# Kernel tuning notes

Measured on AMD Instinct MI355X. Metric: run time of the kernel, lower is better.

The kernel has to match this reference:

```python
import jax, jax.numpy as jnp
import numpy as np

N, E = 50000, 800000
IN_DIM, HID, HEADS, OUT_DIM, NUM_CLASSES = 512, 128, 4, 64, 4


def setup_inputs() -> dict:
    key = jax.random.key(0)
    ks = jax.random.split(key, 18)
    g = lambda k, shape, s=0.05: (jax.random.normal(k, shape, dtype=jnp.float32) * s)
    x = jax.random.normal(ks[0], (N, IN_DIM), dtype=jnp.float32)
    edge_index = jax.random.randint(ks[1], (2, E), 0, N, dtype=jnp.int32)
    return {
        "x": x,
        "edge_index": edge_index,
        # GATConv layer 1 (heads=4, concat)
        "W1": g(ks[2], (IN_DIM, HEADS * HID)),
        "att_src1": g(ks[3], (HEADS, HID)),
        "att_dst1": g(ks[4], (HEADS, HID)),
        "b1": jnp.zeros((HEADS * HID,), jnp.float32),
        # GATConv layer 2 (heads=1, no concat)
        "W2": g(ks[5], (HEADS * HID, OUT_DIM)),
        "att_src2": g(ks[6], (1, OUT_DIM)),
        "att_dst2": g(ks[7], (1, OUT_DIM)),
        "b2": jnp.zeros((OUT_DIM,), jnp.float32),
        # intra_attention MLP: Linear(out,out) -> tanh -> Linear(out,1) -> softmax(dim=0)
        "Wa": g(ks[8], (OUT_DIM, OUT_DIM)),
        "ba": jnp.zeros((OUT_DIM,), jnp.float32),
        "wv": g(ks[9], (OUT_DIM, 1)),
        "bv": jnp.zeros((1,), jnp.float32),
        "class_attn": g(ks[10], (NUM_CLASSES, OUT_DIM), 0.3),
        # classifier
        "Wc": g(ks[11], (OUT_DIM, NUM_CLASSES)),
        "bc": jnp.zeros((NUM_CLASSES,), jnp.float32),
    }


def _gat_layer(x, src, dst, W, att_src, att_dst, heads, feat):
    """PyG GATConv: gather -> LeakyReLU score -> segment softmax -> scatter add."""
    n = x.shape[0]
    h = (x @ W).reshape(n, heads, feat)                     # [N,H,F]
    a_s = jnp.sum(h * att_src[None], axis=-1)               # [N,H]
    a_d = jnp.sum(h * att_dst[None], axis=-1)               # [N,H]
    e = jax.nn.leaky_relu(a_s[src] + a_d[dst], 0.2)         # [E,H]
    m = jax.ops.segment_max(e, dst, num_segments=n)         # per-dst max
    ex = jnp.exp(e - m[dst])
    s = jax.ops.segment_sum(ex, dst, num_segments=n)
    alpha = ex / (s[dst] + 1e-16)                           # [E,H]
    msg = h[src] * alpha[:, :, None]                        # [E,H,F]
    return jax.ops.segment_sum(msg, dst, num_segments=n)    # [N,H,F]


def reference(x, edge_index, W1, att_src1, att_dst1, b1, W2, att_src2, att_dst2,
              b2, Wa, ba, wv, bv, class_attn, Wc, bc):
    n = x.shape[0]
    loop = jnp.arange(n, dtype=edge_index.dtype)
    src = jnp.concatenate([edge_index[0], loop])            # add_self_loops=True
    dst = jnp.concatenate([edge_index[1], loop])

    h1 = _gat_layer(x, src, dst, W1, att_src1, att_dst1, HEADS, HID)
    h1 = h1.reshape(n, HEADS * HID) + b1                    # concat heads + bias
    h1 = jax.nn.elu(h1)

    h2 = _gat_layer(h1, src, dst, W2, att_src2, att_dst2, 1, OUT_DIM)
    h2 = h2.reshape(n, OUT_DIM) + b2                        # heads=1, concat=False

    # intra-sample attention, softmax over nodes (dim=0)
    scores = jnp.tanh(h2 @ Wa + ba) @ wv + bv               # [N,1]
    attw = jax.nn.softmax(scores, axis=0)
    xw = h2 * attw                                          # [N,OUT]

    xn = xw / jnp.maximum(jnp.linalg.norm(xw, axis=1, keepdims=True), 1e-12)
    cn = class_attn / jnp.maximum(
        jnp.linalg.norm(class_attn, axis=1, keepdims=True), 1e-12)
    inter_class_scores = xn @ cn.T                          # [N,C]

    out = xw @ Wc + bc                                      # [N,C]
    return out, xw, inter_class_scores
```

## Files before the change

kernel.cpp:

```cpp
#include <hip/hip_runtime.h>
#include <cstdint>
#include <cstddef>

typedef __attribute__((ext_vector_type(8))) short bf16x8;
typedef __attribute__((ext_vector_type(4))) float f32x4;
typedef __attribute__((ext_vector_type(8))) unsigned short u16x8;

__device__ __forceinline__ unsigned encf(float f) {
  unsigned u = __float_as_uint(f);
  return (u & 0x80000000u) ? ~u : (u | 0x80000000u);
}
__device__ __forceinline__ float decf(unsigned u) {
  return (u & 0x80000000u) ? __uint_as_float(u & 0x7FFFFFFFu) : __uint_as_float(~u);
}
__device__ __forceinline__ float lrelu02(float x) { return x > 0.f ? x : 0.2f * x; }
__device__ __forceinline__ unsigned short f2bf(float f) {
  unsigned u = __float_as_uint(f);
  unsigned r = u + 0x7FFFu + ((u >> 16) & 1u);
  return (unsigned short)(r >> 16);
}
__device__ __forceinline__ float bf2f(unsigned short b) {
  return __uint_as_float(((unsigned)b) << 16);
}

__device__ __forceinline__ void gll16(const void* g, void* l) {
  __builtin_amdgcn_global_load_lds(
      (const __attribute__((address_space(1))) void*)g,
      (__attribute__((address_space(3))) void*)l, 16, 0, 0);
}

__global__ void zero_int_k(int* __restrict__ p, int n) {
  int i = blockIdx.x * 256 + threadIdx.x;
  if (i < n) p[i] = 0;
}

__global__ void hist_k(const int* __restrict__ ei, int E, int N, int* __restrict__ counts) {
  int i = blockIdx.x * 256 + threadIdx.x;
  int Eall = E + N;
  if (i >= Eall) return;
  int dst = (i < E) ? ei[E + i] : (i - E);
  atomicAdd(&counts[dst], 1);
}

__global__ __launch_bounds__(256) void scan1_k(const int* __restrict__ counts,
                                               int* __restrict__ incl,
                                               int* __restrict__ bsum, int N) {
  int b = blockIdx.x, tid = threadIdx.x;
  int lane = tid & 63, wv = tid >> 6;
  int i = b * 256 + tid;
  int v = (i < N) ? counts[i] : 0;
#pragma unroll
  for (int o = 1; o < 64; o <<= 1) {
    int t = __shfl_up(v, o, 64);
    if (lane >= o) v += t;
  }
  __shared__ int wsum[4];
  if (lane == 63) wsum[wv] = v;
  __syncthreads();
  int base = 0;
  for (int wj = 0; wj < wv; wj++) base += wsum[wj];
  v += base;
  if (i < N) incl[i] = v;
  if (tid == 255) bsum[b] = v;
}

__global__ __launch_bounds__(256) void scan2_k(const int* __restrict__ bsum,
                                               int* __restrict__ pb, int nb) {
  int tid = threadIdx.x;
  int lane = tid & 63, wv = tid >> 6;
  int v = (tid < nb) ? bsum[tid] : 0;
  int orig = v;
#pragma unroll
  for (int o = 1; o < 64; o <<= 1) {
    int t = __shfl_up(v, o, 64);
    if (lane >= o) v += t;
  }
  __shared__ int wsum[4];
  if (lane == 63) wsum[wv] = v;
  __syncthreads();
  int base = 0;
  for (int wj = 0; wj < wv; wj++) base += wsum[wj];
  if (tid < nb) pb[tid] = v + base - orig;
}

__global__ void scan3_k(const int* __restrict__ incl, const int* __restrict__ pb,
                        int* __restrict__ offs, int* __restrict__ cursor, int N) {
  int i = blockIdx.x * 256 + threadIdx.x;
  if (i == 0) { offs[0] = 0; cursor[0] = 0; }
  if (i < N) {
    int v = incl[i] + pb[i >> 8];
    offs[i + 1] = v;
    if (i + 1 < N) cursor[i + 1] = v;
  }
}

__global__ void scatter_k(const int* __restrict__ ei, int E, int N,
                          int* __restrict__ cursor, int* __restrict__ ssrc) {
  int i = blockIdx.x * 256 + threadIdx.x;
  int Eall = E + N;
  if (i >= Eall) return;
  int src, dst;
  if (i < E) { src = ei[i]; dst = ei[E + i]; }
  else       { src = i - E; dst = i - E; }
  int pos = atomicAdd(&cursor[dst], 1);
  ssrc[pos] = src;
}

__global__ void conv_x_k(const float* __restrict__ x, unsigned short* __restrict__ xb,
                         int N, int Mpad) {
  int i = blockIdx.x * 256 + threadIdx.x;
  int total = Mpad * 64;
  if (i >= total) return;
  int row = i >> 6;
  u16x8 v;
  if (row < N) {
    const float4* src = (const float4*)(x + (size_t)i * 8);
    float4 a = src[0], b = src[1];
    v[0] = f2bf(a.x); v[1] = f2bf(a.y); v[2] = f2bf(a.z); v[3] = f2bf(a.w);
    v[4] = f2bf(b.x); v[5] = f2bf(b.y); v[6] = f2bf(b.z); v[7] = f2bf(b.w);
  } else {
    v = (u16x8)0;
  }
  *(u16x8*)(xb + (size_t)i * 8) = v;
}

__global__ void conv_wt_k(const float* __restrict__ W, unsigned short* __restrict__ Wt,
                          int K, int Nc) {
  int i = blockIdx.x * 256 + threadIdx.x;
  if (i >= K * Nc) return;
  int c = i / K, k = i - c * K;
  Wt[i] = f2bf(W[(size_t)k * Nc + c]);
}

template <int BM, int BN, bool OBF, bool DOTS>
__global__ __launch_bounds__(256) void mfma_gemm_k(const unsigned short* __restrict__ A,
                                                   const unsigned short* __restrict__ Bt,
                                                   void* __restrict__ Cv,
                                                   const float* __restrict__ att_s,
                                                   const float* __restrict__ att_d,
                                                   float* __restrict__ as_out,
                                                   float* __restrict__ ad_out,
                                                   int M, int K, int Nc) {
  constexpr int BK = 64;
  constexpr int MR = BM / 32;
  constexpr int NR = BN / 32;
  __shared__ unsigned short As[BM][BK];
  __shared__ unsigned short Bs[BN][BK];
  const int tid = threadIdx.x;
  const int lane = tid & 63;
  const int w = tid >> 6;
  const int wr = w >> 1, wc = w & 1;
  const int l16 = lane & 15, lk = lane >> 4;
  const int row0 = blockIdx.x * BM, col0 = blockIdx.y * BN;

  f32x4 acc[MR][NR];
#pragma unroll
  for (int m = 0; m < MR; m++)
#pragma unroll
    for (int n = 0; n < NR; n++) acc[m][n] = (f32x4)0.f;

  const char* Abase = (const char*)A;
  const char* Bbase = (const char*)Bt;

  for (int k0 = 0; k0 < K; k0 += BK) {
#pragma unroll
    for (int i = 0; i < BM / 32; i++) {
      int ca = i * 256 + tid;
      int r = ca >> 3, b = (ca & 7) * 16;
      gll16(Abase + ((size_t)(row0 + r) * K + k0) * 2 + b, (char*)&As[0][0] + ca * 16);
    }
#pragma unroll
    for (int i = 0; i < BN / 32; i++) {
      int cb = i * 256 + tid;
      int c = cb >> 3, b = (cb & 7) * 16;
      gll16(Bbase + ((size_t)(col0 + c) * K + k0) * 2 + b, (char*)&Bs[0][0] + cb * 16);
    }
    __syncthreads();
#pragma unroll
    for (int ks = 0; ks < 2; ks++) {
      bf16x8 af[MR], bfr[NR];
#pragma unroll
      for (int m = 0; m < MR; m++)
        af[m] = *(const bf16x8*)&As[wr * (BM / 2) + m * 16 + l16][ks * 32 + lk * 8];
#pragma unroll
      for (int n = 0; n < NR; n++)
        bfr[n] = *(const bf16x8*)&Bs[wc * (BN / 2) + n * 16 + l16][ks * 32 + lk * 8];
#pragma unroll
      for (int m = 0; m < MR; m++)
#pragma unroll
        for (int n = 0; n < NR; n++)
          acc[m][n] = __builtin_amdgcn_mfma_f32_16x16x32_bf16(af[m], bfr[n], acc[m][n], 0, 0, 0);
    }
    __syncthreads();
  }
#pragma unroll
  for (int m = 0; m < MR; m++) {
    int row_b = row0 + wr * (BM / 2) + m * 16 + lk * 4;
#pragma unroll
    for (int r = 0; r < 4; r++) {
      int row = row_b + r;
      if (row < M) {
#pragma unroll
        for (int n = 0; n < NR; n++) {
          int col = col0 + wc * (BN / 2) + n * 16 + l16;
          if (OBF)
            ((unsigned short*)Cv)[(size_t)row * Nc + col] = f2bf(acc[m][n][r]);
          else
            ((float*)Cv)[(size_t)row * Nc + col] = acc[m][n][r];
        }
      }
    }
  }
  if constexpr (DOTS) {
    __shared__ float s_ds[2][BM];
    __shared__ float s_dd[2][BM];
    float as_c[NR], ad_c[NR];
#pragma unroll
    for (int n = 0; n < NR; n++) {
      int col = col0 + wc * (BN / 2) + n * 16 + l16;
      as_c[n] = att_s[col];
      ad_c[n] = att_d[col];
    }
#pragma unroll
    for (int m = 0; m < MR; m++) {
#pragma unroll
      for (int r = 0; r < 4; r++) {
        float ps = 0.f, pd = 0.f;
#pragma unroll
        for (int n = 0; n < NR; n++) {
          ps += acc[m][n][r] * as_c[n];
          pd += acc[m][n][r] * ad_c[n];
        }
#pragma unroll
        for (int o = 8; o; o >>= 1) { ps += __shfl_xor(ps, o); pd += __shfl_xor(pd, o); }
        if (l16 == 0) {
          int rr = wr * (BM / 2) + m * 16 + lk * 4 + r;
          s_ds[wc][rr] = ps;
          s_dd[wc][rr] = pd;
        }
      }
    }
    __syncthreads();
    if (tid < BM) {
      int row = row0 + tid;
      if (row < M) {
        as_out[(size_t)row * 4 + blockIdx.y] = s_ds[0][tid] + s_ds[1][tid];
        ad_out[(size_t)row * 4 + blockIdx.y] = s_dd[0][tid] + s_dd[1][tid];
      }
    }
  }
}

__global__ __launch_bounds__(256) void attn_dots2_k(const float* __restrict__ h,
                                                    const float* __restrict__ att_s,
                                                    const float* __restrict__ att_d,
                                                    float* __restrict__ a_s,
                                                    float* __restrict__ a_d, int N) {
  int lane = threadIdx.x & 63, wave = threadIdx.x >> 6;
  int n = blockIdx.x * 4 + wave;
  if (n >= N) return;
  float v = h[(size_t)n * 64 + lane];
  float ps = v * att_s[lane], pd = v * att_d[lane];
#pragma unroll
  for (int o = 32; o; o >>= 1) { ps += __shfl_xor(ps, o); pd += __shfl_xor(pd, o); }
  if (lane == 0) { a_s[n] = ps; a_d[n] = pd; }
}

__global__ __launch_bounds__(256) void gat_agg1_k(const unsigned short* __restrict__ hfeat,
                                                  const float* __restrict__ a_s,
                                                  const float* __restrict__ a_d,
                                                  const int* __restrict__ offs,
                                                  const int* __restrict__ ssrc,
                                                  const float* __restrict__ b1,
                                                  unsigned short* __restrict__ h1b, int N) {
  const int tid = threadIdx.x;
  const int lane = tid & 63, wave = tid >> 6;
  const int n = blockIdx.x * 4 + wave;
  if (n >= N) return;
  __shared__ int   s_src[4][64];
  __shared__ float s_ex[4][64][4];
  const int start = offs[n], end = offs[n + 1];
  const int hhl = lane >> 4;
  const float4 adv4 = *(const float4*)(a_d + (size_t)n * 4);
  const float4* as4 = (const float4*)a_s;

  float m0 = -1e30f, m1 = -1e30f, m2 = -1e30f, m3 = -1e30f;
  float S0 = 0.f, S1 = 0.f, S2 = 0.f, S3 = 0.f;
  float acc[8] = {0.f, 0.f, 0.f, 0.f, 0.f, 0.f, 0.f, 0.f};

  for (int base = start; base < end; base += 64) {
    const int cnt = min(64, end - base);
    float e0 = -1e30f, e1 = -1e30f, e2 = -1e30f, e3 = -1e30f;
    int s = 0;
    if (lane < cnt) {
      s = ssrc[base + lane];
      float4 av = as4[s];
      e0 = lrelu02(av.x + adv4.x);
      e1 = lrelu02(av.y + adv4.y);
      e2 = lrelu02(av.z + adv4.z);
      e3 = lrelu02(av.w + adv4.w);
    }
    float c0 = e0, c1 = e1, c2 = e2, c3 = e3;
#pragma unroll
    for (int o = 32; o; o >>= 1) {
      c0 = fmaxf(c0, __shfl_xor(c0, o));
      c1 = fmaxf(c1, __shfl_xor(c1, o));
      c2 = fmaxf(c2, __shfl_xor(c2, o));
      c3 = fmaxf(c3, __shfl_xor(c3, o));
    }
    float nm0 = fmaxf(m0, c0), nm1 = fmaxf(m1, c1);
    float nm2 = fmaxf(m2, c2), nm3 = fmaxf(m3, c3);
    float sc0 = __expf(m0 - nm0), sc1 = __expf(m1 - nm1);
    float sc2 = __expf(m2 - nm2), sc3 = __expf(m3 - nm3);
    m0 = nm0; m1 = nm1; m2 = nm2; m3 = nm3;
    float x0 = (lane < cnt) ? __expf(e0 - nm0) : 0.f;
    float x1 = (lane < cnt) ? __expf(e1 - nm1) : 0.f;
    float x2 = (lane < cnt) ? __expf(e2 - nm2) : 0.f;
    float x3 = (lane < cnt) ? __expf(e3 - nm3) : 0.f;
    s_src[wave][lane] = s;
    s_ex[wave][lane][0] = x0; s_ex[wave][lane][1] = x1;
    s_ex[wave][lane][2] = x2; s_ex[wave][lane][3] = x3;
#pragma unroll
    for (int o = 32; o; o >>= 1) {
      x0 += __shfl_xor(x0, o); x1 += __shfl_xor(x1, o);
      x2 += __shfl_xor(x2, o); x3 += __shfl_xor(x3, o);
    }
    S0 = S0 * sc0 + x0; S1 = S1 * sc1 + x1;
    S2 = S2 * sc2 + x2; S3 = S3 * sc3 + x3;
    float scl = (hhl == 0) ? sc0 : (hhl == 1) ? sc1 : (hhl == 2) ? sc2 : sc3;
#pragma unroll
    for (int q = 0; q < 8; q++) acc[q] *= scl;
#pragma unroll 4
    for (int j = 0; j < cnt; j++) {
      int sj = s_src[wave][j];
      float al = s_ex[wave][j][hhl];
      uint4 pk = *(const uint4*)(hfeat + ((size_t)sj << 9) + lane * 8);
      acc[0] += al * __uint_as_float(pk.x << 16);
      acc[1] += al * __uint_as_float(pk.x & 0xFFFF0000u);
      acc[2] += al * __uint_as_float(pk.y << 16);
      acc[3] += al * __uint_as_float(pk.y & 0xFFFF0000u);
      acc[4] += al * __uint_as_float(pk.z << 16);
      acc[5] += al * __uint_as_float(pk.z & 0xFFFF0000u);
      acc[6] += al * __uint_as_float(pk.w << 16);
      acc[7] += al * __uint_as_float(pk.w & 0xFFFF0000u);
    }
  }
  float inv = 1.f / (((hhl == 0) ? S0 : (hhl == 1) ? S1 : (hhl == 2) ? S2 : S3) + 1e-16f);
  const float4 b1a = *(const float4*)(b1 + lane * 8);
  const float4 b1b = *(const float4*)(b1 + lane * 8 + 4);
  float v[8];
  v[0] = acc[0] * inv + b1a.x; v[1] = acc[1] * inv + b1a.y;
  v[2] = acc[2] * inv + b1a.z; v[3] = acc[3] * inv + b1a.w;
  v[4] = acc[4] * inv + b1b.x; v[5] = acc[5] * inv + b1b.y;
  v[6] = acc[6] * inv + b1b.z; v[7] = acc[7] * inv + b1b.w;
  u16x8 outv;
#pragma unroll
  for (int q = 0; q < 8; q++) {
    float t = v[q] > 0.f ? v[q] : (__expf(v[q]) - 1.f);
    outv[q] = f2bf(t);
  }
  *(u16x8*)(h1b + ((size_t)n << 9) + lane * 8) = outv;
}

__global__ __launch_bounds__(256) void gat_agg2_k(const float* __restrict__ h2pre,
                                                  const float* __restrict__ a_s,
                                                  const float* __restrict__ a_d,
                                                  const int* __restrict__ offs,
                                                  const int* __restrict__ ssrc,
                                                  const float* __restrict__ b2,
                                                  float* __restrict__ h2out, int N) {
  const int tid = threadIdx.x;
  const int lane = tid & 63, wave = tid >> 6;
  const int n = blockIdx.x * 4 + wave;
  if (n >= N) return;
  __shared__ int   s_src[4][64];
  __shared__ float s_ex[4][64];
  const int start = offs[n], end = offs[n + 1];
  const float ad = a_d[n];

  float m = -1e30f, S = 0.f, acc = 0.f;
  for (int base = start; base < end; base += 64) {
    const int cnt = min(64, end - base);
    float e = -1e30f;
    int s = 0;
    if (lane < cnt) {
      s = ssrc[base + lane];
      e = lrelu02(a_s[s] + ad);
    }
    float c = e;
#pragma unroll
    for (int o = 32; o; o >>= 1) c = fmaxf(c, __shfl_xor(c, o));
    float nm = fmaxf(m, c);
    float sc = __expf(m - nm);
    m = nm;
    float x = (lane < cnt) ? __expf(e - nm) : 0.f;
    s_src[wave][lane] = s;
    s_ex[wave][lane] = x;
#pragma unroll
    for (int o = 32; o; o >>= 1) x += __shfl_xor(x, o);
    S = S * sc + x;
    acc *= sc;
#pragma unroll 4
    for (int j = 0; j < cnt; j++) {
      int sj = s_src[wave][j];
      float al = s_ex[wave][j];
      acc += al * h2pre[((size_t)sj << 6) + lane];
    }
  }
  h2out[((size_t)n << 6) + lane] = acc / (S + 1e-16f) + b2[lane];
}

__global__ __launch_bounds__(256) void score_k(const float* __restrict__ h2,
                                               const float* __restrict__ Wa,
                                               const float* __restrict__ ba,
                                               const float* __restrict__ wv,
                                               const float* __restrict__ bv,
                                               float* __restrict__ scores, int N) {
  int lane = threadIdx.x & 63, wave = threadIdx.x >> 6;
  int n = blockIdx.x * 4 + wave;
  if (n >= N) return;
  float hv = h2[(size_t)n * 64 + lane];
  float t = ba[lane];
  for (int k = 0; k < 64; k++) {
    float hk = __shfl(hv, k);
    t += hk * Wa[k * 64 + lane];
  }
  t = tanhf(t);
  float p = t * wv[lane];
#pragma unroll
  for (int o = 32; o; o >>= 1) p += __shfl_xor(p, o);
  if (lane == 0) scores[n] = p + bv[0];
}

__global__ void red_init_k(unsigned* __restrict__ red) {
  if (threadIdx.x == 0) { red[0] = 0x007FFFFFu; red[1] = 0u; }
}

__global__ void score_max_k(const float* __restrict__ scores, unsigned* __restrict__ red, int N) {
  int i = blockIdx.x * 256 + threadIdx.x;
  float m = (i < N) ? scores[i] : -1e30f;
#pragma unroll
  for (int o = 32; o; o >>= 1) m = fmaxf(m, __shfl_xor(m, o));
  if ((threadIdx.x & 63) == 0) atomicMax(&red[0], encf(m));
}

__global__ void score_sum_k(const float* __restrict__ scores, unsigned* __restrict__ red, int N) {
  float M = decf(red[0]);
  int i = blockIdx.x * 256 + threadIdx.x;
  float s = (i < N) ? __expf(scores[i] - M) : 0.f;
#pragma unroll
  for (int o = 32; o; o >>= 1) s += __shfl_xor(s, o);
  if ((threadIdx.x & 63) == 0) atomicAdd(reinterpret_cast<float*>(red) + 1, s);
}

__global__ void prep_cn_k(const float* __restrict__ ca, float* __restrict__ cn) {
  int lane = threadIdx.x & 63, c = threadIdx.x >> 6;
  float v = ca[c * 64 + lane];
  float p = v * v;
#pragma unroll
  for (int o = 32; o; o >>= 1) p += __shfl_xor(p, o);
  cn[c * 64 + lane] = v / fmaxf(sqrtf(p), 1e-12f);
}

__global__ __launch_bounds__(256) void finalize_k(const float* __restrict__ h2,
                                                  const float* __restrict__ scores,
                                                  const unsigned* __restrict__ red,
                                                  const float* __restrict__ cn,
                                                  const float* __restrict__ Wc,
                                                  const float* __restrict__ bc,
                                                  float* __restrict__ out, int N) {
  int lane = threadIdx.x & 63, wave = threadIdx.x >> 6;
  int n = blockIdx.x * 4 + wave;
  if (n >= N) return;
  float M = decf(red[0]);
  float S = __uint_as_float(red[1]);
  float attw = __expf(scores[n] - M) / S;
  float xw = h2[(size_t)n * 64 + lane] * attw;
  float p = xw * xw;
#pragma unroll
  for (int o = 32; o; o >>= 1) p += __shfl_xor(p, o);
  float xn = xw / fmaxf(sqrtf(p), 1e-12f);
  float i0 = xn * cn[lane],       i1 = xn * cn[64 + lane];
  float i2 = xn * cn[128 + lane], i3 = xn * cn[192 + lane];
  float o0 = xw * Wc[lane * 4 + 0], o1 = xw * Wc[lane * 4 + 1];
  float o2 = xw * Wc[lane * 4 + 2], o3 = xw * Wc[lane * 4 + 3];
#pragma unroll
  for (int o = 32; o; o >>= 1) {
    i0 += __shfl_xor(i0, o); i1 += __shfl_xor(i1, o);
    i2 += __shfl_xor(i2, o); i3 += __shfl_xor(i3, o);
    o0 += __shfl_xor(o0, o); o1 += __shfl_xor(o1, o);
    o2 += __shfl_xor(o2, o); o3 += __shfl_xor(o3, o);
  }
  float* outp   = out;
  float* xwp    = out + (size_t)N * 4;
  float* interp = out + (size_t)N * 68;
  xwp[(size_t)n * 64 + lane] = xw;
  if (lane == 0) {
    outp[n * 4 + 0] = o0 + bc[0]; outp[n * 4 + 1] = o1 + bc[1];
    outp[n * 4 + 2] = o2 + bc[2]; outp[n * 4 + 3] = o3 + bc[3];
    interp[n * 4 + 0] = i0; interp[n * 4 + 1] = i1;
    interp[n * 4 + 2] = i2; interp[n * 4 + 3] = i3;
  }
}

extern "C" void kernel_launch(void* const* d_in, const int* in_sizes, int n_in,
                              void* d_out, int out_size, void* d_ws, size_t ws_size,
                              hipStream_t stream) {
  const float* x        = (const float*)d_in[0];
  const int*   ei       = (const int*)d_in[1];
  const float* W1       = (const float*)d_in[2];
  const float* att_src1 = (const float*)d_in[3];
  const float* att_dst1 = (const float*)d_in[4];
  const float* b1       = (const float*)d_in[5];
  const float* W2       = (const float*)d_in[6];
  const float* att_src2 = (const float*)d_in[7];
  const float* att_dst2 = (const float*)d_in[8];
  const float* b2       = (const float*)d_in[9];
  const float* Wa       = (const float*)d_in[10];
  const float* ba       = (const float*)d_in[11];
  const float* wv       = (const float*)d_in[12];
  const float* bv       = (const float*)d_in[13];
  const float* class_attn = (const float*)d_in[14];
  const float* Wc       = (const float*)d_in[15];
  const float* bc       = (const float*)d_in[16];

  const int N = in_sizes[0] / 512;
  const int E = in_sizes[1] / 2;
  const int Eall = E + N;
  const int Mpad = ((N + 127) / 128) * 128;
  const int nb = (N + 255) / 256;

  char* w = (char*)d_ws;
  size_t off = 0;
  auto alloc = [&](size_t bytes) -> void* {
    off = (off + 255) & ~((size_t)255);
    void* p = w + off;
    off += bytes;
    return p;
  };
  unsigned short* xb  = (unsigned short*)alloc((size_t)Mpad * 512 * 2);
  unsigned short* h1b = xb;
  unsigned short* hb  = (unsigned short*)alloc((size_t)N * 512 * 2);
  float* h2pre  = (float*)alloc((size_t)N * 64 * 4);
  float* h2     = (float*)alloc((size_t)N * 64 * 4);
  unsigned short* W1t = (unsigned short*)alloc((size_t)512 * 512 * 2);
  unsigned short* W2t = (unsigned short*)alloc((size_t)64 * 512 * 2);
  float* as1    = (float*)alloc((size_t)N * 4 * 4);
  float* ad1    = (float*)alloc((size_t)N * 4 * 4);
  float* as2    = (float*)alloc((size_t)N * 4);
  float* ad2    = (float*)alloc((size_t)N * 4);
  int*   counts = (int*)alloc((size_t)N * 4);
  int*   incl   = (int*)alloc((size_t)N * 4);
  int*   bsum   = (int*)alloc(256 * 4);
  int*   pb     = (int*)alloc(256 * 4);
  int*   offs   = (int*)alloc((size_t)(N + 1) * 4);
  int*   cursor = (int*)alloc((size_t)N * 4);
  int*   ssrc   = (int*)alloc((size_t)Eall * 4);
  float* scores = (float*)alloc((size_t)N * 4);
  unsigned* red = (unsigned*)alloc(64);
  float* cn     = (float*)alloc(256 * 4);

  const int gN256  = (N + 255) / 256;
  const int gE256  = (Eall + 255) / 256;
  const int gNode4 = (N + 3) / 4;

  zero_int_k<<<gN256, 256, 0, stream>>>(counts, N);
  hist_k<<<gE256, 256, 0, stream>>>(ei, E, N, counts);
  scan1_k<<<nb, 256, 0, stream>>>(counts, incl, bsum, N);
  scan2_k<<<1, 256, 0, stream>>>(bsum, pb, nb);
  scan3_k<<<gN256, 256, 0, stream>>>(incl, pb, offs, cursor, N);
  scatter_k<<<gE256, 256, 0, stream>>>(ei, E, N, cursor, ssrc);

  conv_x_k<<<(Mpad * 64 + 255) / 256, 256, 0, stream>>>(x, xb, N, Mpad);
  conv_wt_k<<<(512 * 512 + 255) / 256, 256, 0, stream>>>(W1, W1t, 512, 512);
  conv_wt_k<<<(64 * 512 + 255) / 256, 256, 0, stream>>>(W2, W2t, 512, 64);

  mfma_gemm_k<128, 128, true, true><<<dim3(Mpad / 128, 4), 256, 0, stream>>>(
      xb, W1t, hb, att_src1, att_dst1, as1, ad1, N, 512, 512);
  gat_agg1_k<<<gNode4, 256, 0, stream>>>(hb, as1, ad1, offs, ssrc, b1, h1b, N);

  mfma_gemm_k<64, 64, false, false><<<dim3(Mpad / 64, 1), 256, 0, stream>>>(
      h1b, W2t, h2pre, nullptr, nullptr, nullptr, nullptr, N, 512, 64);
  attn_dots2_k<<<gNode4, 256, 0, stream>>>(h2pre, att_src2, att_dst2, as2, ad2, N);
  gat_agg2_k<<<gNode4, 256, 0, stream>>>(h2pre, as2, ad2, offs, ssrc, b2, h2, N);

  score_k<<<gNode4, 256, 0, stream>>>(h2, Wa, ba, wv, bv, scores, N);
  red_init_k<<<1, 64, 0, stream>>>(red);
  score_max_k<<<gN256, 256, 0, stream>>>(scores, red, N);
  score_sum_k<<<gN256, 256, 0, stream>>>(scores, red, N);
  prep_cn_k<<<1, 256, 0, stream>>>(class_attn, cn);
  finalize_k<<<gNode4, 256, 0, stream>>>(h2, scores, red, cn, Wc, bc,
                                         (float*)d_out, N);
}
```

Baseline: 481.6 us.

## Widen GEMM1 tile, fuse layer-2 attention dots into GEMM2, store h2 in bf16

GEMM1 now uses a 128x256 tile, so each block covers two heads and writes per-head dot products directly, halving the grid's column dimension and reusing A tiles more. GEMM2 gets a specialised kernel that computes the att_src/att_dst dots in its epilogue, which removes the separate attn_dots2 pass. It also writes h2pre as bf16, and gat_agg2 splits edges across wave halves with packed bf16 pair loads. This cuts gather bandwidth in the second aggregation, at the cost of bf16 rounding of h2pre and higher register and LDS use in GEMM1.

```diff
diff --git a/kernel.cpp b/kernel.cpp
--- a/kernel.cpp
+++ b/kernel.cpp
@@ -132,45 +132,43 @@
   Wt[i] = f2bf(W[(size_t)k * Nc + c]);
 }
 
-template <int BM, int BN, bool OBF, bool DOTS>
-__global__ __launch_bounds__(256) void mfma_gemm_k(const unsigned short* __restrict__ A,
-                                                   const unsigned short* __restrict__ Bt,
-                                                   void* __restrict__ Cv,
-                                                   const float* __restrict__ att_s,
-                                                   const float* __restrict__ att_d,
-                                                   float* __restrict__ as_out,
-                                                   float* __restrict__ ad_out,
-                                                   int M, int K, int Nc) {
-  constexpr int BK = 64;
-  constexpr int MR = BM / 32;
-  constexpr int NR = BN / 32;
-  __shared__ unsigned short As[BM][BK];
-  __shared__ unsigned short Bs[BN][BK];
+__global__ __launch_bounds__(256, 2) void gemm1_k(const unsigned short* __restrict__ A,
+                                                  const unsigned short* __restrict__ Bt,
+                                                  unsigned short* __restrict__ C,
+                                                  const float* __restrict__ att_s,
+                                                  const float* __restrict__ att_d,
+                                                  float* __restrict__ as_out,
+                                                  float* __restrict__ ad_out,
+                                                  int M, int K, int Nc) {
+  __shared__ unsigned short As[128][64];
+  __shared__ unsigned short Bs[256][64];
+  __shared__ float s_ds[2][128];
+  __shared__ float s_dd[2][128];
   const int tid = threadIdx.x;
   const int lane = tid & 63;
   const int w = tid >> 6;
   const int wr = w >> 1, wc = w & 1;
   const int l16 = lane & 15, lk = lane >> 4;
-  const int row0 = blockIdx.x * BM, col0 = blockIdx.y * BN;
-
-  f32x4 acc[MR][NR];
-#pragma unroll
-  for (int m = 0; m < MR; m++)
-#pragma unroll
-    for (int n = 0; n < NR; n++) acc[m][n] = (f32x4)0.f;
+  const int row0 = blockIdx.x * 128, col0 = blockIdx.y * 256;
+
+  f32x4 acc[4][8];
+#pragma unroll
+  for (int m = 0; m < 4; m++)
+#pragma unroll
+    for (int n = 0; n < 8; n++) acc[m][n] = (f32x4)0.f;
 
   const char* Abase = (const char*)A;
   const char* Bbase = (const char*)Bt;
 
-  for (int k0 = 0; k0 < K; k0 += BK) {
-#pragma unroll
-    for (int i = 0; i < BM / 32; i++) {
+  for (int k0 = 0; k0 < K; k0 += 64) {
+#pragma unroll
+    for (int i = 0; i < 4; i++) {
       int ca = i * 256 + tid;
       int r = ca >> 3, b = (ca & 7) * 16;
       gll16(Abase + ((size_t)(row0 + r) * K + k0) * 2 + b, (char*)&As[0][0] + ca * 16);
     }
 #pragma unroll
-    for (int i = 0; i < BN / 32; i++) {
+    for (int i = 0; i < 8; i++) {
       int cb = i * 256 + tid;
       int c = cb >> 3, b = (cb & 7) * 16;
       gll16(Bbase + ((size_t)(col0 + c) * K + k0) * 2 + b, (char*)&Bs[0][0] + cb * 16);
@@ -178,92 +176,183 @@
     __syncthreads();
 #pragma unroll
     for (int ks = 0; ks < 2; ks++) {
-      bf16x8 af[MR], bfr[NR];
-#pragma unroll
-      for (int m = 0; m < MR; m++)
-        af[m] = *(const bf16x8*)&As[wr * (BM / 2) + m * 16 + l16][ks * 32 + lk * 8];
-#pragma unroll
-      for (int n = 0; n < NR; n++)
-        bfr[n] = *(const bf16x8*)&Bs[wc * (BN / 2) + n * 16 + l16][ks * 32 + lk * 8];
-#pragma unroll
-      for (int m = 0; m < MR; m++)
-#pragma unroll
-        for (int n = 0; n < NR; n++)
+      bf16x8 af[4], bfr[8];
+#pragma unroll
+      for (int m = 0; m < 4; m++)
+        af[m] = *(const bf16x8*)&As[wr * 64 + m * 16 + l16][ks * 32 + lk * 8];
+#pragma unroll
+      for (int n = 0; n < 8; n++)
+        bfr[n] = *(const bf16x8*)&Bs[wc * 128 + n * 16 + l16][ks * 32 + lk * 8];
+#pragma unroll
+      for (int m = 0; m < 4; m++)
+#pragma unroll
+        for (int n = 0; n < 8; n++)
           acc[m][n] = __builtin_amdgcn_mfma_f32_16x16x32_bf16(af[m], bfr[n], acc[m][n], 0, 0, 0);
     }
     __syncthreads();
   }
 #pragma unroll
-  for (int m = 0; m < MR; m++) {
-    int row_b = row0 + wr * (BM / 2) + m * 16 + lk * 4;
+  for (int m = 0; m < 4; m++) {
+    int row_b = row0 + wr * 64 + m * 16 + lk * 4;
 #pragma unroll
     for (int r = 0; r < 4; r++) {
       int row = row_b + r;
       if (row < M) {
 #pragma unroll
-        for (int n = 0; n < NR; n++) {
-          int col = col0 + wc * (BN / 2) + n * 16 + l16;
-          if (OBF)
-            ((unsigned short*)Cv)[(size_t)row * Nc + col] = f2bf(acc[m][n][r]);
-          else
-            ((float*)Cv)[(size_t)row * Nc + col] = acc[m][n][r];
+        for (int n = 0; n < 8; n++) {
+          int col = col0 + wc * 128 + n * 16 + l16;
+          C[(size_t)row * Nc + col] = f2bf(acc[m][n][r]);
         }
       }
     }
   }
-  if constexpr (DOTS) {
-    __shared__ float s_ds[2][BM];
-    __shared__ float s_dd[2][BM];
-    float as_c[NR], ad_c[NR];
-#pragma unroll
-    for (int n = 0; n < NR; n++) {
-      int col = col0 + wc * (BN / 2) + n * 16 + l16;
-      as_c[n] = att_s[col];
-      ad_c[n] = att_d[col];
-    }
-#pragma unroll
-    for (int m = 0; m < MR; m++) {
-#pragma unroll
-      for (int r = 0; r < 4; r++) {
-        float ps = 0.f, pd = 0.f;
-#pragma unroll
-        for (int n = 0; n < NR; n++) {
-          ps += acc[m][n][r] * as_c[n];
-          pd += acc[m][n][r] * ad_c[n];
-        }
-#pragma unroll
-        for (int o = 8; o; o >>= 1) { ps += __shfl_xor(ps, o); pd += __shfl_xor(pd, o); }
-        if (l16 == 0) {
-          int rr = wr * (BM / 2) + m * 16 + lk * 4 + r;
-          s_ds[wc][rr] = ps;
-          s_dd[wc][rr] = pd;
+  float as_c[8], ad_c[8];
+#pragma unroll
+  for (int n = 0; n < 8; n++) {
+    int col = col0 + wc * 128 + n * 16 + l16;
+    as_c[n] = att_s[col];
+    ad_c[n] = att_d[col];
+  }
+#pragma unroll
+  for (int m = 0; m < 4; m++) {
+#pragma unroll
+    for (int r = 0; r < 4; r++) {
+      float ps = 0.f, pd = 0.f;
+#pragma unroll
+      for (int n = 0; n < 8; n++) {
+        ps += acc[m][n][r] * as_c[n];
+        pd += acc[m][n][r] * ad_c[n];
+      }
+#pragma unroll
+      for (int o = 8; o; o >>= 1) { ps += __shfl_xor(ps, o); pd += __shfl_xor(pd, o); }
+      if (l16 == 0) {
+        int rr = wr * 64 + m * 16 + lk * 4 + r;
+        s_ds[wc][rr] = ps;
+        s_dd[wc][rr] = pd;
+      }
+    }
+  }
+  __syncthreads();
+  if (tid < 128) {
+    int row = row0 + tid;
+    if (row < M) {
+      int hb = 2 * blockIdx.y;
+      as_out[(size_t)row * 4 + hb + 0] = s_ds[0][tid];
+      as_out[(size_t)row * 4 + hb + 1] = s_ds[1][tid];
+      ad_out[(size_t)row * 4 + hb + 0] = s_dd[0][tid];
+      ad_out[(size_t)row * 4 + hb + 1] = s_dd[1][tid];
+    }
+  }
+}
+
+__global__ __launch_bounds__(256) void gemm2_k(const unsigned short* __restrict__ A,
+                                               const unsigned short* __restrict__ Bt,
+                                               unsigned short* __restrict__ C,
+                                               const float* __restrict__ att_s,
+                                               const float* __restrict__ att_d,
+                                               float* __restrict__ as_out,
+                                               float* __restrict__ ad_out,
+                                               int M, int K, int Nc) {
+  __shared__ unsigned short As[64][64];
+  __shared__ unsigned short Bs[64][64];
+  __shared__ float s_ds[2][64];
+  __shared__ float s_dd[2][64];
+  const int tid = threadIdx.x;
+  const int lane = tid & 63;
+  const int w = tid >> 6;
+  const int wr = w >> 1, wc = w & 1;
+  const int l16 = lane & 15, lk = lane >> 4;
+  const int row0 = blockIdx.x * 64;
+
+  f32x4 acc[2][2];
+#pragma unroll
+  for (int m = 0; m < 2; m++)
+#pragma unroll
+    for (int n = 0; n < 2; n++) acc[m][n] = (f32x4)0.f;
+
+  const char* Abase = (const char*)A;
+  const char* Bbase = (const char*)Bt;
+
+  for (int k0 = 0; k0 < K; k0 += 64) {
+#pragma unroll
+    for (int i = 0; i < 2; i++) {
+      int ca = i * 256 + tid;
+      int r = ca >> 3, b = (ca & 7) * 16;
+      gll16(Abase + ((size_t)(row0 + r) * K + k0) * 2 + b, (char*)&As[0][0] + ca * 16);
+    }
+#pragma unroll
+    for (int i = 0; i < 2; i++) {
+      int cb = i * 256 + tid;
+      int c = cb >> 3, b = (cb & 7) * 16;
+      gll16(Bbase + ((size_t)c * K + k0) * 2 + b, (char*)&Bs[0][0] + cb * 16);
+    }
+    __syncthreads();
+#pragma unroll
+    for (int ks = 0; ks < 2; ks++) {
+      bf16x8 af[2], bfr[2];
+#pragma unroll
+      for (int m = 0; m < 2; m++)
+        af[m] = *(const bf16x8*)&As[wr * 32 + m * 16 + l16][ks * 32 + lk * 8];
+#pragma unroll
+      for (int n = 0; n < 2; n++)
+        bfr[n] = *(const bf16x8*)&Bs[wc * 32 + n * 16 + l16][ks * 32 + lk * 8];
+#pragma unroll
+      for (int m = 0; m < 2; m++)
+#pragma unroll
+        for (int n = 0; n < 2; n++)
+          acc[m][n] = __builtin_amdgcn_mfma_f32_16x16x32_bf16(af[m], bfr[n], acc[m][n], 0, 0, 0);
+    }
+    __syncthreads();
+  }
+#pragma unroll
+  for (int m = 0; m < 2; m++) {
+    int row_b = row0 + wr * 32 + m * 16 + lk * 4;
+#pragma unroll
+    for (int r = 0; r < 4; r++) {
+      int row = row_b + r;
+      if (row < M) {
+#pragma unroll
+        for (int n = 0; n < 2; n++) {
+          int col = wc * 32 + n * 16 + l16;
+          C[(size_t)row * Nc + col] = f2bf(acc[m][n][r]);
         }
       }
     }
-    __syncthreads();
-    if (tid < BM) {
-      int row = row0 + tid;
-      if (row < M) {
-        as_out[(size_t)row * 4 + blockIdx.y] = s_ds[0][tid] + s_ds[1][tid];
-        ad_out[(size_t)row * 4 + blockIdx.y] = s_dd[0][tid] + s_dd[1][tid];
+  }
+  float as_c[2], ad_c[2];
+#pragma unroll
+  for (int n = 0; n < 2; n++) {
+    int col = wc * 32 + n * 16 + l16;
+    as_c[n] = att_s[col];
+    ad_c[n] = att_d[col];
+  }
+#pragma unroll
+  for (int m = 0; m < 2; m++) {
+#pragma unroll
+    for (int r = 0; r < 4; r++) {
+      float ps = 0.f, pd = 0.f;
+#pragma unroll
+      for (int n = 0; n < 2; n++) {
+        ps += acc[m][n][r] * as_c[n];
+        pd += acc[m][n][r] * ad_c[n];
       }
-    }
-  }
-}
-
-__global__ __launch_bounds__(256) void attn_dots2_k(const float* __restrict__ h,
-                                                    const float* __restrict__ att_s,
-                                                    const float* __restrict__ att_d,
-                                                    float* __restrict__ a_s,
-                                                    float* __restrict__ a_d, int N) {
-  int lane = threadIdx.x & 63, wave = threadIdx.x >> 6;
-  int n = blockIdx.x * 4 + wave;
-  if (n >= N) return;
-  float v = h[(size_t)n * 64 + lane];
-  float ps = v * att_s[lane], pd = v * att_d[lane];
-#pragma unroll
-  for (int o = 32; o; o >>= 1) { ps += __shfl_xor(ps, o); pd += __shfl_xor(pd, o); }
-  if (lane == 0) { a_s[n] = ps; a_d[n] = pd; }
+#pragma unroll
+      for (int o = 8; o; o >>= 1) { ps += __shfl_xor(ps, o); pd += __shfl_xor(pd, o); }
+      if (l16 == 0) {
+        int rr = wr * 32 + m * 16 + lk * 4 + r;
+        s_ds[wc][rr] = ps;
+        s_dd[wc][rr] = pd;
+      }
+    }
+  }
+  __syncthreads();
+  if (tid < 64) {
+    int row = row0 + tid;
+    if (row < M) {
+      as_out[row] = s_ds[0][tid] + s_ds[1][tid];
+      ad_out[row] = s_dd[0][tid] + s_dd[1][tid];
+    }
+  }
 }
 
 __global__ __launch_bounds__(256) void gat_agg1_k(const unsigned short* __restrict__ hfeat,
@@ -362,7 +451,7 @@
   *(u16x8*)(h1b + ((size_t)n << 9) + lane * 8) = outv;
 }
 
-__global__ __launch_bounds__(256) void gat_agg2_k(const float* __restrict__ h2pre,
+__global__ __launch_bounds__(256) void gat_agg2_k(const unsigned short* __restrict__ h2b,
                                                   const float* __restrict__ a_s,
                                                   const float* __restrict__ a_d,
                                                   const int* __restrict__ offs,
@@ -377,8 +466,9 @@
   __shared__ float s_ex[4][64];
   const int start = offs[n], end = offs[n + 1];
   const float ad = a_d[n];
-
-  float m = -1e30f, S = 0.f, acc = 0.f;
+  const int half = lane >> 5, l32 = lane & 31;
+
+  float m = -1e30f, S = 0.f, acc0 = 0.f, acc1 = 0.f;
   for (int base = start; base < end; base += 64) {
     const int cnt = min(64, end - base);
     float e = -1e30f;
@@ -396,18 +486,29 @@
     float x = (lane < cnt) ? __expf(e - nm) : 0.f;
     s_src[wave][lane] = s;
     s_ex[wave][lane] = x;
-#pragma unroll
-    for (int o = 32; o; o >>= 1) x += __shfl_xor(x, o);
-    S = S * sc + x;
-    acc *= sc;
+    float xs = x;
+#pragma unroll
+    for (int o = 32; o; o >>= 1) xs += __shfl_xor(xs, o);
+    S = S * sc + xs;
+    acc0 *= sc; acc1 *= sc;
 #pragma unroll 4
-    for (int j = 0; j < cnt; j++) {
+    for (int j = half; j < cnt; j += 2) {
       int sj = s_src[wave][j];
       float al = s_ex[wave][j];
-      acc += al * h2pre[((size_t)sj << 6) + lane];
-    }
-  }
-  h2out[((size_t)n << 6) + lane] = acc / (S + 1e-16f) + b2[lane];
+      unsigned pk = *(const unsigned*)(h2b + ((size_t)sj << 6) + l32 * 2);
+      acc0 += al * __uint_as_float(pk << 16);
+      acc1 += al * __uint_as_float(pk & 0xFFFF0000u);
+    }
+  }
+  acc0 += __shfl_xor(acc0, 32);
+  acc1 += __shfl_xor(acc1, 32);
+  if (half == 0) {
+    float inv = 1.f / (S + 1e-16f);
+    float2 o;
+    o.x = acc0 * inv + b2[l32 * 2];
+    o.y = acc1 * inv + b2[l32 * 2 + 1];
+    *(float2*)(h2out + ((size_t)n << 6) + l32 * 2) = o;
+  }
 }
 
 __global__ __launch_bounds__(256) void score_k(const float* __restrict__ h2,
@@ -541,7 +642,7 @@
   unsigned short* xb  = (unsigned short*)alloc((size_t)Mpad * 512 * 2);
   unsigned short* h1b = xb;
   unsigned short* hb  = (unsigned short*)alloc((size_t)N * 512 * 2);
-  float* h2pre  = (float*)alloc((size_t)N * 64 * 4);
+  unsigned short* h2b = (unsigned short*)alloc((size_t)N * 64 * 2);
   float* h2     = (float*)alloc((size_t)N * 64 * 4);
   unsigned short* W1t = (unsigned short*)alloc((size_t)512 * 512 * 2);
   unsigned short* W2t = (unsigned short*)alloc((size_t)64 * 512 * 2);
@@ -575,14 +676,13 @@
   conv_wt_k<<<(512 * 512 + 255) / 256, 256, 0, stream>>>(W1, W1t, 512, 512);
   conv_wt_k<<<(64 * 512 + 255) / 256, 256, 0, stream>>>(W2, W2t, 512, 64);
 
-  mfma_gemm_k<128, 128, true, true><<<dim3(Mpad / 128, 4), 256, 0, stream>>>(
+  gemm1_k<<<dim3(Mpad / 128, 2), 256, 0, stream>>>(
       xb, W1t, hb, att_src1, att_dst1, as1, ad1, N, 512, 512);
   gat_agg1_k<<<gNode4, 256, 0, stream>>>(hb, as1, ad1, offs, ssrc, b1, h1b, N);
 
-  mfma_gemm_k<64, 64, false, false><<<dim3(Mpad / 64, 1), 256, 0, stream>>>(
-      h1b, W2t, h2pre, nullptr, nullptr, nullptr, nullptr, N, 512, 64);
-  attn_dots2_k<<<gNode4, 256, 0, stream>>>(h2pre, att_src2, att_dst2, as2, ad2, N);
-  gat_agg2_k<<<gNode4, 256, 0, stream>>>(h2pre, as2, ad2, offs, ssrc, b2, h2, N);
+  gemm2_k<<<dim3(Mpad / 64, 1), 256, 0, stream>>>(
+      h1b, W2t, h2b, att_src2, att_dst2, as2, ad2, N, 512, 64);
+  gat_agg2_k<<<gNode4, 256, 0, stream>>>(h2b, as2, ad2, offs, ssrc, b2, h2, N);
 
   score_k<<<gNode4, 256, 0, stream>>>(h2, Wa, ba, wv, bv, scores, N);
   red_init_k<<<1, 64, 0, stream>>>(red);
```

New measurement: 444.5 us. -7.7%, faster.
